# Performance work log

Measured on AMD Instinct MI355X. Metric: run time of the kernel, lower is better.

## Reference

```python
import jax, jax.numpy as jnp
import numpy as np

D = 1024

def setup_inputs() -> dict:
    key = jax.random.key(0)
    kx, kw = jax.random.split(key)
    x = jax.random.normal(kx, (4, 2048, D), dtype=jnp.float32)
    # nn.Linear(d, 3d, bias=False): weight [3d, d]; y = x @ W.T
    W = jax.random.normal(kw, (3 * D, D), dtype=jnp.float32) * (1.0 / np.sqrt(D))
    return {"x": x, "W": W}

def reference(x, W):
    d = x.shape[-1]
    qkv = jnp.einsum('bsd,ed->bse', x, W)  # [B,S,3d]
    q, k, v = jnp.split(qkv, 3, axis=2)
    att = jnp.einsum('bqd,bkd->bqk', q, k) * (1.0 / jnp.sqrt(jnp.asarray(d, x.dtype)))
    att = jax.nn.softmax(att, axis=-1)
    y = jnp.einsum('bqk,bkd->bqd', att, v)
    return y
```

## Files before the change

kernel.cpp:

```cpp
#include <hip/hip_runtime.h>
#include <hip/hip_bf16.h>

typedef __attribute__((ext_vector_type(8))) short short8;
typedef __attribute__((ext_vector_type(4))) float f32x4;

typedef unsigned short u16;

__device__ __forceinline__ u16 f32_to_bf16(float f) {
    unsigned int u = __float_as_uint(f);
    u += 0x7fffu + ((u >> 16) & 1u);
    return (u16)(u >> 16);
}
__device__ __forceinline__ float bf16_to_f32(u16 h) {
    return __uint_as_float(((unsigned int)h) << 16);
}

__device__ __forceinline__ void gload16(const u16* g, u16* lds_base) {
    __builtin_amdgcn_global_load_lds(
        (const __attribute__((address_space(1))) void*)g,
        (__attribute__((address_space(3))) void*)lds_base, 16, 0, 0);
}

__global__ void cast_inputs(const float* __restrict__ x, u16* __restrict__ Xb,
                            const float* __restrict__ W, u16* __restrict__ Wb,
                            int nx4, int nw4) {
    int i = blockIdx.x * blockDim.x + threadIdx.x;
    const float* in; u16* out; int idx;
    if (i < nx4) { in = x; out = Xb; idx = i; }
    else { idx = i - nx4; if (idx >= nw4) return; in = W; out = Wb; }
    float4 v = ((const float4*)in)[idx];
    ushort4 o;
    o.x = f32_to_bf16(v.x); o.y = f32_to_bf16(v.y);
    o.z = f32_to_bf16(v.z); o.w = f32_to_bf16(v.w);
    ((ushort4*)out)[idx] = o;
}

struct GemmFrag {
    f32x4 acc[4][4];
    int wm, wn, lane;
};

__device__ __forceinline__ void gemm_core_128(
    const u16* __restrict__ A, const u16* __restrict__ Bt, int K, int lda, int ldb,
    int row0, int col0, u16* sA, u16* sB, GemmFrag& fr)
{
    const int t    = threadIdx.x;
    const int lane = t & 63;
    const int wave = t >> 6;
    fr.lane = lane;
    fr.wm = (wave >> 1) * 64;
    fr.wn = (wave & 1) * 64;
    const int lr = lane & 15;

#pragma unroll
    for (int i = 0; i < 4; ++i)
#pragma unroll
        for (int j = 0; j < 4; ++j)
            fr.acc[i][j] = (f32x4){0.f, 0.f, 0.f, 0.f};

    const int srow = lane >> 3;
    const int gc   = (lane & 7) ^ srow;
    for (int k0 = 0; k0 < K; k0 += 64) {
        __syncthreads();
#pragma unroll
        for (int c = 0; c < 4; ++c) {
            const int rb = c * 32 + wave * 8;
            const int r  = rb + srow;
            gload16(A  + (long long)(row0 + r) * lda + k0 + gc * 8, &sA[rb * 64]);
            gload16(Bt + (long long)(col0 + r) * ldb + k0 + gc * 8, &sB[rb * 64]);
        }
        __syncthreads();

#pragma unroll
        for (int kk = 0; kk < 64; kk += 32) {
            const int cb = (lane >> 4) + (kk >> 3);
            const int sl = (cb ^ (lr & 7)) * 8;
            short8 af[4], bf[4];
#pragma unroll
            for (int i = 0; i < 4; ++i) {
                af[i] = *(const short8*)(&sA[(fr.wm + i * 16 + lr) * 64 + sl]);
                bf[i] = *(const short8*)(&sB[(fr.wn + i * 16 + lr) * 64 + sl]);
            }
#pragma unroll
            for (int i = 0; i < 4; ++i)
#pragma unroll
                for (int j = 0; j < 4; ++j)
                    fr.acc[i][j] = __builtin_amdgcn_mfma_f32_16x16x32_bf16(
                        af[i], bf[j], fr.acc[i][j], 0, 0, 0);
        }
    }
}

__global__ __launch_bounds__(256) void gemm_qkv(
    const u16* __restrict__ Xb, const u16* __restrict__ Wb,
    u16* __restrict__ QKV, u16* __restrict__ VT)
{
    __shared__ u16 sA[128 * 64];
    __shared__ u16 sB[128 * 64];
    const int row0 = blockIdx.y * 128;
    const int col0 = blockIdx.x * 128;
    GemmFrag fr;
    gemm_core_128(Xb, Wb, 1024, 1024, 1024, row0, col0, sA, sB, fr);

    const int cr = (fr.lane >> 4) * 4;
    const int cc = fr.lane & 15;
    if (col0 < 2048) {
#pragma unroll
        for (int i = 0; i < 4; ++i)
#pragma unroll
            for (int j = 0; j < 4; ++j)
#pragma unroll
                for (int r = 0; r < 4; ++r) {
                    int grow = row0 + fr.wm + i * 16 + cr + r;
                    int gcol = col0 + fr.wn + j * 16 + cc;
                    QKV[(long long)grow * 3072 + gcol] = f32_to_bf16(fr.acc[i][j][r]);
                }
    } else {
#pragma unroll
        for (int i = 0; i < 4; ++i) {
            int grow = row0 + fr.wm + i * 16 + cr;
            int b = grow >> 11, s = grow & 2047;
#pragma unroll
            for (int j = 0; j < 4; ++j) {
                int d = col0 - 2048 + fr.wn + j * 16 + cc;
                ushort4 o;
                o.x = f32_to_bf16(fr.acc[i][j][0]);
                o.y = f32_to_bf16(fr.acc[i][j][1]);
                o.z = f32_to_bf16(fr.acc[i][j][2]);
                o.w = f32_to_bf16(fr.acc[i][j][3]);
                *(ushort4*)(&VT[((long long)(b * 1024 + d)) * 2048 + s]) = o;
            }
        }
    }
}

__global__ __launch_bounds__(256) void gemm_s(
    const u16* __restrict__ QKV, u16* __restrict__ S)
{
    __shared__ u16 sA[128 * 64];
    __shared__ u16 sB[128 * 64];
    const long long boff = (long long)blockIdx.z * 2048 * 3072;
    const u16* Q = QKV + boff;
    const u16* K = QKV + boff + 1024;
    u16* Sb = S + (long long)blockIdx.z * 2048 * 2048;
    const int row0 = blockIdx.y * 128;
    const int col0 = blockIdx.x * 128;
    GemmFrag fr;
    gemm_core_128(Q, K, 1024, 3072, 3072, row0, col0, sA, sB, fr);

    const int cr = (fr.lane >> 4) * 4;
    const int cc = fr.lane & 15;
#pragma unroll
    for (int i = 0; i < 4; ++i)
#pragma unroll
        for (int j = 0; j < 4; ++j)
#pragma unroll
            for (int r = 0; r < 4; ++r) {
                int grow = row0 + fr.wm + i * 16 + cr + r;
                int gcol = col0 + fr.wn + j * 16 + cc;
                Sb[(long long)grow * 2048 + gcol] = f32_to_bf16(fr.acc[i][j][r]);
            }
}

__global__ __launch_bounds__(256) void gemm_pv(
    const u16* __restrict__ P, const u16* __restrict__ VT,
    float* __restrict__ Y)
{
    __shared__ u16 sA[128 * 64];
    __shared__ u16 sB[128 * 64];
    const u16* Pb  = P  + (long long)blockIdx.z * 2048 * 2048;
    const u16* VTb = VT + (long long)blockIdx.z * 1024 * 2048;
    float* Yb = Y + (long long)blockIdx.z * 2048 * 1024;
    const int row0 = blockIdx.y * 128;
    const int col0 = blockIdx.x * 128;
    GemmFrag fr;
    gemm_core_128(Pb, VTb, 2048, 2048, 2048, row0, col0, sA, sB, fr);

    const int cr = (fr.lane >> 4) * 4;
    const int cc = fr.lane & 15;
#pragma unroll
    for (int i = 0; i < 4; ++i)
#pragma unroll
        for (int j = 0; j < 4; ++j)
#pragma unroll
            for (int r = 0; r < 4; ++r) {
                int grow = row0 + fr.wm + i * 16 + cr + r;
                int gcol = col0 + fr.wn + j * 16 + cc;
                Yb[(long long)grow * 1024 + gcol] = fr.acc[i][j][r];
            }
}

__global__ __launch_bounds__(256) void softmax_rows(
    const u16* __restrict__ S, u16* __restrict__ P, float scale)
{
    const long long row = blockIdx.x;
    const u16* s = S + row * 2048;
    u16* p = P + row * 2048;
    const int t = threadIdx.x;
    const int lane = t & 63, w = t >> 6;

    short8 raw = *(const short8*)(s + t * 8);
    float v[8];
    float m = -1e30f;
#pragma unroll
    for (int i = 0; i < 8; ++i) {
        v[i] = bf16_to_f32((u16)raw[i]) * scale;
        m = fmaxf(m, v[i]);
    }
#pragma unroll
    for (int off = 32; off > 0; off >>= 1) m = fmaxf(m, __shfl_xor(m, off, 64));
    __shared__ float sm[4], ss[4];
    if (lane == 0) sm[w] = m;
    __syncthreads();
    m = fmaxf(fmaxf(sm[0], sm[1]), fmaxf(sm[2], sm[3]));

    float sum = 0.f;
#pragma unroll
    for (int i = 0; i < 8; ++i) {
        v[i] = __expf(v[i] - m);
        sum += v[i];
    }
#pragma unroll
    for (int off = 32; off > 0; off >>= 1) sum += __shfl_xor(sum, off, 64);
    if (lane == 0) ss[w] = sum;
    __syncthreads();
    const float inv = 1.0f / (ss[0] + ss[1] + ss[2] + ss[3]);
    short8 o;
#pragma unroll
    for (int i = 0; i < 8; ++i) o[i] = (short)f32_to_bf16(v[i] * inv);
    *(short8*)(p + t * 8) = o;
}

extern "C" void kernel_launch(void* const* d_in, const int* in_sizes, int n_in,
                              void* d_out, int out_size, void* d_ws, size_t ws_size,
                              hipStream_t stream) {
    const float* x = (const float*)d_in[0];
    const float* W = (const float*)d_in[1];
    float* out = (float*)d_out;

    char* ws = (char*)d_ws;
    u16*   Xb  = (u16*)(ws);
    u16*   Wb  = (u16*)(ws + 16777216LL);
    u16*   QKV = (u16*)(ws + 23068672LL);
    u16*   VT  = (u16*)(ws + 73400320LL);
    u16*   P   = (u16*)(ws + 90177536LL);
    u16*   S   = (u16*)(ws + 123731968LL);

    const bool batched = (ws_size >= 123731968ULL + 33554432ULL);

    cast_inputs<<<11264, 256, 0, stream>>>(x, Xb, W, Wb,
                                           8192 * 1024 / 4, 3072 * 1024 / 4);

    gemm_qkv<<<dim3(24, 64, 1), 256, 0, stream>>>(Xb, Wb, QKV, VT);

    if (batched) {
        gemm_s<<<dim3(16, 16, 4), 256, 0, stream>>>(QKV, S);
        softmax_rows<<<8192, 256, 0, stream>>>(S, P, 0.03125f);
    } else {
        for (int b = 0; b < 4; ++b) {
            gemm_s<<<dim3(16, 16, 1), 256, 0, stream>>>(
                QKV + (long long)b * 2048 * 3072 - (long long)b * 2048 * 3072 + (long long)b * 2048 * 3072,
                S);
            softmax_rows<<<2048, 256, 0, stream>>>(
                S, P + (long long)b * 2048 * 2048, 0.03125f);
        }
    }

    gemm_pv<<<dim3(8, 16, 4), 256, 0, stream>>>(P, VT, out);
}
```

Baseline: 267.4 us.

## Split QKV projection into QK and V GEMMs, use 128x64 tiles for V and PV

Splits the fused QKV projection into a QK GEMM with 128x128 tiles and a separate V GEMM that writes V transposed, using a new 128x64 tile core. The PV GEMM also moves to 128x64 tiles, doubling its grid from 512 to 1024 blocks so the GPU's compute units are filled better. The QK buffer is compacted to a 2048-wide row stride, and the unbatched fallback path is dropped. In exchange, the smaller tiles lower operand reuse per block and add one extra kernel launch.

```diff
diff --git a/kernel.cpp b/kernel.cpp
--- a/kernel.cpp
+++ b/kernel.cpp
@@ -35,14 +35,12 @@
     ((ushort4*)out)[idx] = o;
 }
 
-struct GemmFrag {
-    f32x4 acc[4][4];
-    int wm, wn, lane;
-};
+
+struct Frag128 { f32x4 acc[4][4]; int lane, wm, wn; };
 
 __device__ __forceinline__ void gemm_core_128(
     const u16* __restrict__ A, const u16* __restrict__ Bt, int K, int lda, int ldb,
-    int row0, int col0, u16* sA, u16* sB, GemmFrag& fr)
+    int row0, int col0, u16* sA, u16* sB, Frag128& fr)
 {
     const int t    = threadIdx.x;
     const int lane = t & 63;
@@ -91,62 +89,131 @@
     }
 }
 
-__global__ __launch_bounds__(256) void gemm_qkv(
-    const u16* __restrict__ Xb, const u16* __restrict__ Wb,
-    u16* __restrict__ QKV, u16* __restrict__ VT)
+struct FragN64 { f32x4 acc[2][4]; int lane, wm; };
+
+__device__ __forceinline__ void gemm_core_n64(
+    const u16* __restrict__ A, const u16* __restrict__ Bt, int K, int lda, int ldb,
+    int row0, int col0, u16* sA, u16* sB, FragN64& fr)
+{
+    const int t    = threadIdx.x;
+    const int lane = t & 63;
+    const int wave = t >> 6;
+    fr.lane = lane;
+    fr.wm = wave * 32;
+    const int lr = lane & 15;
+
+#pragma unroll
+    for (int i = 0; i < 2; ++i)
+#pragma unroll
+        for (int j = 0; j < 4; ++j)
+            fr.acc[i][j] = (f32x4){0.f, 0.f, 0.f, 0.f};
+
+    const int srow = lane >> 3;
+    const int gc   = (lane & 7) ^ srow;
+    for (int k0 = 0; k0 < K; k0 += 64) {
+        __syncthreads();
+#pragma unroll
+        for (int c = 0; c < 4; ++c) {
+            const int rb = c * 32 + wave * 8;
+            gload16(A + (long long)(row0 + rb + srow) * lda + k0 + gc * 8,
+                    &sA[rb * 64]);
+        }
+#pragma unroll
+        for (int c = 0; c < 2; ++c) {
+            const int rb = c * 32 + wave * 8;
+            gload16(Bt + (long long)(col0 + rb + srow) * ldb + k0 + gc * 8,
+                    &sB[rb * 64]);
+        }
+        __syncthreads();
+
+#pragma unroll
+        for (int kk = 0; kk < 64; kk += 32) {
+            const int cb = (lane >> 4) + (kk >> 3);
+            const int sl = (cb ^ (lr & 7)) * 8;
+            short8 af[2], bf[4];
+#pragma unroll
+            for (int i = 0; i < 2; ++i)
+                af[i] = *(const short8*)(&sA[(fr.wm + i * 16 + lr) * 64 + sl]);
+#pragma unroll
+            for (int j = 0; j < 4; ++j)
+                bf[j] = *(const short8*)(&sB[(j * 16 + lr) * 64 + sl]);
+#pragma unroll
+            for (int i = 0; i < 2; ++i)
+#pragma unroll
+                for (int j = 0; j < 4; ++j)
+                    fr.acc[i][j] = __builtin_amdgcn_mfma_f32_16x16x32_bf16(
+                        af[i], bf[j], fr.acc[i][j], 0, 0, 0);
+        }
+    }
+}
+
+
+__global__ __launch_bounds__(256) void gemm_qk(
+    const u16* __restrict__ Xb, const u16* __restrict__ Wb, u16* __restrict__ QK)
 {
     __shared__ u16 sA[128 * 64];
     __shared__ u16 sB[128 * 64];
     const int row0 = blockIdx.y * 128;
     const int col0 = blockIdx.x * 128;
-    GemmFrag fr;
+    Frag128 fr;
     gemm_core_128(Xb, Wb, 1024, 1024, 1024, row0, col0, sA, sB, fr);
 
     const int cr = (fr.lane >> 4) * 4;
     const int cc = fr.lane & 15;
-    if (col0 < 2048) {
-#pragma unroll
-        for (int i = 0; i < 4; ++i)
-#pragma unroll
-            for (int j = 0; j < 4; ++j)
-#pragma unroll
-                for (int r = 0; r < 4; ++r) {
-                    int grow = row0 + fr.wm + i * 16 + cr + r;
-                    int gcol = col0 + fr.wn + j * 16 + cc;
-                    QKV[(long long)grow * 3072 + gcol] = f32_to_bf16(fr.acc[i][j][r]);
-                }
-    } else {
-#pragma unroll
-        for (int i = 0; i < 4; ++i) {
-            int grow = row0 + fr.wm + i * 16 + cr;
-            int b = grow >> 11, s = grow & 2047;
-#pragma unroll
-            for (int j = 0; j < 4; ++j) {
-                int d = col0 - 2048 + fr.wn + j * 16 + cc;
-                ushort4 o;
-                o.x = f32_to_bf16(fr.acc[i][j][0]);
-                o.y = f32_to_bf16(fr.acc[i][j][1]);
-                o.z = f32_to_bf16(fr.acc[i][j][2]);
-                o.w = f32_to_bf16(fr.acc[i][j][3]);
-                *(ushort4*)(&VT[((long long)(b * 1024 + d)) * 2048 + s]) = o;
+#pragma unroll
+    for (int i = 0; i < 4; ++i)
+#pragma unroll
+        for (int j = 0; j < 4; ++j)
+#pragma unroll
+            for (int r = 0; r < 4; ++r) {
+                int grow = row0 + fr.wm + i * 16 + cr + r;
+                int gcol = col0 + fr.wn + j * 16 + cc;
+                QK[(long long)grow * 2048 + gcol] = f32_to_bf16(fr.acc[i][j][r]);
             }
+}
+
+__global__ __launch_bounds__(256) void gemm_v(
+    const u16* __restrict__ Xb, const u16* __restrict__ Wv, u16* __restrict__ VT)
+{
+    __shared__ u16 sA[128 * 64];
+    __shared__ u16 sB[64 * 64];
+    const int row0 = blockIdx.y * 128;
+    const int col0 = blockIdx.x * 64;
+    FragN64 fr;
+    gemm_core_n64(Xb, Wv, 1024, 1024, 1024, row0, col0, sA, sB, fr);
+
+    const int cr = (fr.lane >> 4) * 4;
+    const int cc = fr.lane & 15;
+#pragma unroll
+    for (int i = 0; i < 2; ++i) {
+        int grow = row0 + fr.wm + i * 16 + cr;
+        int b = grow >> 11, s = grow & 2047;
+#pragma unroll
+        for (int j = 0; j < 4; ++j) {
+            int d = col0 + j * 16 + cc;
+            ushort4 o;
+            o.x = f32_to_bf16(fr.acc[i][j][0]);
+            o.y = f32_to_bf16(fr.acc[i][j][1]);
+            o.z = f32_to_bf16(fr.acc[i][j][2]);
+            o.w = f32_to_bf16(fr.acc[i][j][3]);
+            *(ushort4*)(&VT[((long long)(b * 1024 + d)) * 2048 + s]) = o;
         }
     }
 }
 
 __global__ __launch_bounds__(256) void gemm_s(
-    const u16* __restrict__ QKV, u16* __restrict__ S)
+    const u16* __restrict__ QK, u16* __restrict__ S)
 {
     __shared__ u16 sA[128 * 64];
     __shared__ u16 sB[128 * 64];
-    const long long boff = (long long)blockIdx.z * 2048 * 3072;
-    const u16* Q = QKV + boff;
-    const u16* K = QKV + boff + 1024;
-    u16* Sb = S + (long long)blockIdx.z * 2048 * 2048;
+    const long long boff = (long long)blockIdx.z * 2048 * 2048;
+    const u16* Q  = QK + boff;
+    const u16* Kp = QK + boff + 1024;
+    u16* Sb = S + boff;
     const int row0 = blockIdx.y * 128;
     const int col0 = blockIdx.x * 128;
-    GemmFrag fr;
-    gemm_core_128(Q, K, 1024, 3072, 3072, row0, col0, sA, sB, fr);
+    Frag128 fr;
+    gemm_core_128(Q, Kp, 1024, 2048, 2048, row0, col0, sA, sB, fr);
 
     const int cr = (fr.lane >> 4) * 4;
     const int cc = fr.lane & 15;
@@ -163,29 +230,28 @@
 }
 
 __global__ __launch_bounds__(256) void gemm_pv(
-    const u16* __restrict__ P, const u16* __restrict__ VT,
-    float* __restrict__ Y)
+    const u16* __restrict__ P, const u16* __restrict__ VT, float* __restrict__ Y)
 {
     __shared__ u16 sA[128 * 64];
-    __shared__ u16 sB[128 * 64];
+    __shared__ u16 sB[64 * 64];
     const u16* Pb  = P  + (long long)blockIdx.z * 2048 * 2048;
     const u16* VTb = VT + (long long)blockIdx.z * 1024 * 2048;
     float* Yb = Y + (long long)blockIdx.z * 2048 * 1024;
     const int row0 = blockIdx.y * 128;
-    const int col0 = blockIdx.x * 128;
-    GemmFrag fr;
-    gemm_core_128(Pb, VTb, 2048, 2048, 2048, row0, col0, sA, sB, fr);
+    const int col0 = blockIdx.x * 64;
+    FragN64 fr;
+    gemm_core_n64(Pb, VTb, 2048, 2048, 2048, row0, col0, sA, sB, fr);
 
     const int cr = (fr.lane >> 4) * 4;
     const int cc = fr.lane & 15;
 #pragma unroll
-    for (int i = 0; i < 4; ++i)
+    for (int i = 0; i < 2; ++i)
 #pragma unroll
         for (int j = 0; j < 4; ++j)
 #pragma unroll
             for (int r = 0; r < 4; ++r) {
                 int grow = row0 + fr.wm + i * 16 + cr + r;
-                int gcol = col0 + fr.wn + j * 16 + cc;
+                int gcol = col0 + j * 16 + cc;
                 Yb[(long long)grow * 1024 + gcol] = fr.acc[i][j][r];
             }
 }
@@ -239,32 +305,21 @@
     float* out = (float*)d_out;
 
     char* ws = (char*)d_ws;
-    u16*   Xb  = (u16*)(ws);
-    u16*   Wb  = (u16*)(ws + 16777216LL);
-    u16*   QKV = (u16*)(ws + 23068672LL);
-    u16*   VT  = (u16*)(ws + 73400320LL);
-    u16*   P   = (u16*)(ws + 90177536LL);
-    u16*   S   = (u16*)(ws + 123731968LL);
-
-    const bool batched = (ws_size >= 123731968ULL + 33554432ULL);
+    u16* Xb = (u16*)(ws);
+    u16* Wb = (u16*)(ws + 16777216LL);
+    u16* QK = (u16*)(ws + 23068672LL);
+    u16* VT = (u16*)(ws + 56623104LL);
+    u16* P  = (u16*)(ws + 73400320LL);
+    u16* S  = (u16*)(ws + 106954752LL);
 
     cast_inputs<<<11264, 256, 0, stream>>>(x, Xb, W, Wb,
                                            8192 * 1024 / 4, 3072 * 1024 / 4);
 
-    gemm_qkv<<<dim3(24, 64, 1), 256, 0, stream>>>(Xb, Wb, QKV, VT);
-
-    if (batched) {
-        gemm_s<<<dim3(16, 16, 4), 256, 0, stream>>>(QKV, S);
-        softmax_rows<<<8192, 256, 0, stream>>>(S, P, 0.03125f);
-    } else {
-        for (int b = 0; b < 4; ++b) {
-            gemm_s<<<dim3(16, 16, 1), 256, 0, stream>>>(
-                QKV + (long long)b * 2048 * 3072 - (long long)b * 2048 * 3072 + (long long)b * 2048 * 3072,
-                S);
-            softmax_rows<<<2048, 256, 0, stream>>>(
-                S, P + (long long)b * 2048 * 2048, 0.03125f);
-        }
-    }
-
-    gemm_pv<<<dim3(8, 16, 4), 256, 0, stream>>>(P, VT, out);
-}
+    gemm_qk<<<dim3(16, 64, 1), 256, 0, stream>>>(Xb, Wb, QK);
+    gemm_v<<<dim3(16, 64, 1), 256, 0, stream>>>(Xb, Wb + 2048 * 1024, VT);
+
+    gemm_s<<<dim3(16, 16, 4), 256, 0, stream>>>(QK, S);
+    softmax_rows<<<8192, 256, 0, stream>>>(S, P, 0.03125f);
+
+    gemm_pv<<<dim3(16, 16, 4), 256, 0, stream>>>(P, VT, out);
+}
```

Measured after the change: 273.9 us. 2.4% more time.
